# Optimization experiments

Measured on AMD Instinct MI355X. Metric: run time of the kernel, lower is better.

## Reference

```python
import jax, jax.numpy as jnp
import numpy as np

T = 32768       # sequence length (batch=1 in original forward)
DY = 63         # mark dim; input_size = DY + 1 = 64
D_IN = 64
H = 256         # hidden_size
OUT = 32        # out_size
NI = 1024       # number of inducing points


def _lstm_scan(x, w_ih, w_hh, b_ih, b_hh, reverse):
    """Single-direction LSTM over [T, D] input, batch=1. PyTorch gate order i,f,g,o."""
    xg = x @ w_ih.T + (b_ih + b_hh)  # [T, 4H], input projection precomputed

    def step(carry, xg_t):
        h, c = carry
        g = xg_t + h @ w_hh.T
        i, f, gg, o = jnp.split(g, 4)
        c = jax.nn.sigmoid(f) * c + jax.nn.sigmoid(i) * jnp.tanh(gg)
        h = jax.nn.sigmoid(o) * jnp.tanh(c)
        return (h, c), h

    init = (jnp.zeros((H,), x.dtype), jnp.zeros((H,), x.dtype))
    _, hs = jax.lax.scan(step, init, xg, reverse=reverse)
    return hs  # [T, H]


def _bilstm(x, layer_params):
    for (wf, uf, bif, bhf, wb, ub, bib, bhb) in layer_params:
        hf = _lstm_scan(x, wf, uf, bif, bhf, False)
        hb = _lstm_scan(x, wb, ub, bib, bhb, True)
        x = jnp.concatenate([hf, hb], axis=-1)  # [T, 2H]
    return x


def setup_inputs() -> dict:
    key = jax.random.key(0)
    ks = iter(jax.random.split(key, 24))
    s = 1.0 / np.sqrt(H)  # PyTorch LSTM uniform(-1/sqrt(H), 1/sqrt(H)) init
    def U(shape):
        return jax.random.uniform(next(ks), shape, jnp.float32, -s, s)
    inp = {
        "Y": jax.random.normal(next(ks), (T, DY), jnp.float32),
        "dT": jax.random.uniform(next(ks), (T,), jnp.float32),
        "induce_idx": jnp.sort(jax.random.randint(next(ks), (NI,), 0, T)),
        # layer 0: input D_IN; layer 1: input 2H (bidirectional)
        "w_ih_l0f": U((4 * H, D_IN)), "w_hh_l0f": U((4 * H, H)), "b_ih_l0f": U((4 * H,)), "b_hh_l0f": U((4 * H,)),
        "w_ih_l0b": U((4 * H, D_IN)), "w_hh_l0b": U((4 * H, H)), "b_ih_l0b": U((4 * H,)), "b_hh_l0b": U((4 * H,)),
        "w_ih_l1f": U((4 * H, 2 * H)), "w_hh_l1f": U((4 * H, H)), "b_ih_l1f": U((4 * H,)), "b_hh_l1f": U((4 * H,)),
        "w_ih_l1b": U((4 * H, 2 * H)), "w_hh_l1b": U((4 * H, H)), "b_ih_l1b": U((4 * H,)), "b_hh_l1b": U((4 * H,)),
        "fc_weight": jax.random.normal(next(ks), (2 * H, 2 * OUT), jnp.float32),
    }
    return inp


def reference(Y, dT, induce_idx,
              w_ih_l0f, w_hh_l0f, b_ih_l0f, b_hh_l0f,
              w_ih_l0b, w_hh_l0b, b_ih_l0b, b_hh_l0b,
              w_ih_l1f, w_hh_l1f, b_ih_l1f, b_hh_l1f,
              w_ih_l1b, w_hh_l1b, b_ih_l1b, b_hh_l1b,
              fc_weight):
    x = jnp.concatenate([Y, dT[:, None]], axis=1)  # [T, D_IN]
    layer_params = [
        (w_ih_l0f, w_hh_l0f, b_ih_l0f, b_hh_l0f, w_ih_l0b, w_hh_l0b, b_ih_l0b, b_hh_l0b),
        (w_ih_l1f, w_hh_l1f, b_ih_l1f, b_hh_l1f, w_ih_l1b, w_hh_l1b, b_ih_l1b, b_hh_l1b),
    ]
    h = _bilstm(x, layer_params)          # [T, 2H]
    out = h @ fc_weight                    # [T, 2*OUT]
    sel = out[induce_idx]                  # [NI, 2*OUT]
    return sel[:, :OUT], sel[:, OUT:]
```

## Files before the change

### kernel.cpp

```cpp
#include <hip/hip_runtime.h>

typedef unsigned int u32;
typedef unsigned short u16;
typedef _Float16 f16;
typedef _Float16 f16x2 __attribute__((ext_vector_type(2)));

#define T_SEQ 32768

static const size_t OFF_DT   = 0;
static const size_t OFF_FLG  = 1024;
static const size_t OFF_MAP  = 4096;
static const size_t OFF_H1G  = 135168;
static const size_t OFF_BIAS = 1183744;
static const size_t OFF_FCW  = 1200128;
static const size_t OFF_WQ8  = 1331200;
static const size_t OFF_WIH0 = 3428352;
static const size_t OFF_WIH1 = 3690496;
static const size_t OFF_XQ   = 5787648;
static const size_t OFF_H0   = 9981952;
static const size_t OFF_XG   = 43536384;
static const size_t XG_DIR   = (size_t)T_SEQ * 1024 * 2;
static const size_t NEED_PAR = OFF_XG + 2 * XG_DIR;

__device__ __forceinline__ float bf2f(u16 u) {
  union { u32 i; float f; } v; v.i = ((u32)u) << 16; return v.f;
}
__device__ __forceinline__ u16 f2bf(float f) {
  union { float f; u32 i; } v; v.f = f;
  u32 u = v.i;
  return (u16)((u + 0x7fffu + ((u >> 16) & 1u)) >> 16);
}
__device__ __forceinline__ u32 packf2(float a, float b) {
  f16x2 p; p.x = (f16)a; p.y = (f16)b;
  return __builtin_bit_cast(u32, p);
}
__device__ __forceinline__ u32 bf2f2(u32 v) {
  union { u32 i; float f; } lo, hi;
  lo.i = v << 16; hi.i = v & 0xffff0000u;
  return packf2(lo.f, hi.f);
}
__device__ __forceinline__ float ldf(const void* p, size_t i, u32 isf) {
  return isf ? ((const float*)p)[i] : bf2f(((const u16*)p)[i]);
}
__device__ __forceinline__ float fdot2f(f16x2 a, f16x2 b, float c) {
#if __has_builtin(__builtin_amdgcn_fdot2)
  return __builtin_amdgcn_fdot2(a, b, c, false);
#else
  return c + (float)a.x * (float)b.x + (float)a.y * (float)b.y;
#endif
}
__device__ __forceinline__ float fdotu(u32 a, u32 b, float c) {
  return fdot2f(__builtin_bit_cast(f16x2, a), __builtin_bit_cast(f16x2, b), c);
}
__device__ __forceinline__ int sdot4(u32 a, u32 b, int c) {
#if __has_builtin(__builtin_amdgcn_sdot4)
  return __builtin_amdgcn_sdot4((int)a, (int)b, c, false);
#else
  int r = c;
#pragma unroll
  for (int j = 0; j < 4; ++j)
    r += (int)(signed char)(a >> (8 * j)) * (int)(signed char)(b >> (8 * j));
  return r;
#endif
}
__device__ __forceinline__ int dpp_xor1(int x) {
#if __has_builtin(__builtin_amdgcn_update_dpp)
  return __builtin_amdgcn_update_dpp(0, x, 0xB1, 0xF, 0xF, true);
#else
  return __shfl_xor(x, 1);
#endif
}
__device__ __forceinline__ float sigf(float x) {
  return __builtin_amdgcn_rcpf(1.0f + __builtin_amdgcn_exp2f(-1.4426950408889634f * x));
}
__device__ __forceinline__ float tanhf_fast(float x) {
  return 1.0f - 2.0f * __builtin_amdgcn_rcpf(1.0f + __builtin_amdgcn_exp2f(2.8853900817779268f * x));
}

__global__ void k_detect(const u16* __restrict__ probe, u32* __restrict__ dt) {
  __shared__ int cnt;
  if (threadIdx.x == 0) cnt = 0;
  __syncthreads();
  int bad = 0;
  for (int i = threadIdx.x; i < 8192; i += 256) {
    float v = bf2f(probe[i]);
    if (!(v * v <= 16.0f)) bad++;
  }
  atomicAdd(&cnt, bad);
  __syncthreads();
  if (threadIdx.x == 0) *dt = (cnt > 64) ? 1u : 0u;
}

__global__ void k_conv_pairs(const void* __restrict__ src, u32* __restrict__ dst,
                             int np, const u32* __restrict__ dtp) {
  u32 isf = *dtp;
  int i = blockIdx.x * 256 + threadIdx.x;
  if (i >= np) return;
  if (isf) {
    const float* s = (const float*)src;
    dst[i] = packf2(s[2 * i], s[2 * i + 1]);
  } else {
    dst[i] = bf2f2(((const u32*)src)[i]);
  }
}

__global__ void k_quant(const void* __restrict__ src, u32* __restrict__ dst,
                        const u32* __restrict__ dtp) {
  u32 isf = *dtp;
  int i = blockIdx.x * 256 + threadIdx.x;
  int row = i >> 6, c = i & 63;
  u32 out = 0;
#pragma unroll
  for (int j = 0; j < 4; ++j) {
    float w = ldf(src, (size_t)row * 256 + 4 * c + j, isf);
    int q = (int)rintf(w * 2048.0f);
    q = q > 127 ? 127 : (q < -127 ? -127 : q);
    out |= ((u32)(q & 0xff)) << (8 * j);
  }
  dst[i] = out;
}

__global__ void k_conv_misc(const void* bi0f, const void* bh0f, const void* bi0b, const void* bh0b,
                            const void* bi1f, const void* bh1f, const void* bi1b, const void* bh1b,
                            const void* fcb, float* __restrict__ bias, float* __restrict__ fcw,
                            u32* __restrict__ flags, int* __restrict__ map,
                            const u32* __restrict__ dtp) {
  u32 isf = *dtp;
  int i = blockIdx.x * 256 + threadIdx.x;
  if (i < 4096) {
    int ld = i >> 10, r = i & 1023;
    const void* bi; const void* bh;
    if (ld == 0)      { bi = bi0f; bh = bh0f; }
    else if (ld == 1) { bi = bi0b; bh = bh0b; }
    else if (ld == 2) { bi = bi1f; bh = bh1f; }
    else              { bi = bi1b; bh = bh1b; }
    bias[i] = ldf(bi, r, isf) + ldf(bh, r, isf);
  } else if (i < 36864) {
    fcw[i - 4096] = ldf(fcb, i - 4096, isf);
  } else if (i < 36992) {
    flags[i - 36864] = 0;
  } else if (i < 69760) {
    map[i - 36992] = -1;
  }
}

__global__ void k_conv_x(const void* __restrict__ Y, const void* __restrict__ dT,
                         u32* __restrict__ xq, const u32* __restrict__ dtp) {
  u32 isf = *dtp;
  int i = blockIdx.x * 256 + threadIdx.x;
  if (i >= T_SEQ * 32) return;
  int t = i >> 5, m = i & 31, k2 = 2 * m;
  float a = ldf(Y, (size_t)t * 63 + k2, isf);
  float b = (k2 + 1 < 63) ? ldf(Y, (size_t)t * 63 + k2 + 1, isf) : ldf(dT, t, isf);
  xq[i] = packf2(a, b);
}

__global__ void k_map_set(const int* __restrict__ idx, int* __restrict__ map) {
  int i = blockIdx.x * 256 + threadIdx.x;
  if (i < 1024) map[idx[i]] = i;
}

__global__ __launch_bounds__(256) void k_gemm(
    const u32* __restrict__ Aq, const u32* __restrict__ Wc,
    const float* __restrict__ bias, f16* __restrict__ xg_slot, int Kp) {
  int t0 = blockIdx.x << 6, r0 = blockIdx.y << 6;
  int tid = threadIdx.x, tx = tid & 15, ty = tid >> 4;
  __shared__ u32 As[64][33];
  __shared__ u32 Bs[64][33];
  float acc[4][4] = {};
  for (int kp0 = 0; kp0 < Kp; kp0 += 32) {
#pragma unroll
    for (int i = 0; i < 8; ++i) {
      int idx = tid + (i << 8);
      int row = idx >> 5, kp = idx & 31, kpg = kp0 + kp;
      As[row][kp] = Aq[(size_t)(t0 + row) * Kp + kpg];
      Bs[row][kp] = Wc[(size_t)(r0 + row) * Kp + kpg];
    }
    __syncthreads();
#pragma unroll 4
    for (int kk = 0; kk < 32; ++kk) {
      u32 av[4], bv[4];
#pragma unroll
      for (int i = 0; i < 4; ++i) av[i] = As[ty * 4 + i][kk];
#pragma unroll
      for (int i = 0; i < 4; ++i) bv[i] = Bs[tx * 4 + i][kk];
#pragma unroll
      for (int i = 0; i < 4; ++i)
#pragma unroll
        for (int j = 0; j < 4; ++j)
          acc[i][j] = fdotu(av[i], bv[j], acc[i][j]);
    }
    __syncthreads();
  }
#pragma unroll
  for (int i = 0; i < 4; ++i) {
    int t = t0 + ty * 4 + i;
#pragma unroll
    for (int j = 0; j < 4; ++j) {
      int r = r0 + tx * 4 + j;
      xg_slot[(size_t)t * 1024 + r] = (f16)(acc[i][j] + bias[r]);
    }
  }
}

__global__ __launch_bounds__(512, 2) void k_recur2(
    const f16* __restrict__ xg, const u32* __restrict__ wq,
    f16* __restrict__ h_full, f16* __restrict__ h1g,
    const int* __restrict__ map, int dir0) {
  const int dir = dir0 + blockIdx.x;
  const int tid = threadIdx.x;
  const int u = tid >> 1;
  const int half = tid & 1;
  const u32* wqd = wq + ((size_t)dir << 16);

  __shared__ __align__(16) unsigned char hb8[2][256];

  u32 w0[32], w1[32], w2[32], w3[32];
  {
    const u32* p0 = wqd + ((size_t)(0 * 256 + u) << 6) + (half << 5);
    const u32* p1 = wqd + ((size_t)(1 * 256 + u) << 6) + (half << 5);
    const u32* p2 = wqd + ((size_t)(2 * 256 + u) << 6) + (half << 5);
    const u32* p3 = wqd + ((size_t)(3 * 256 + u) << 6) + (half << 5);
#pragma unroll
    for (int i = 0; i < 32; ++i) {
      w0[i] = p0[i]; w1[i] = p1[i]; w2[i] = p2[i]; w3[i] = p3[i];
    }
  }
#pragma unroll
  for (int i = 0; i < 32; ++i)
    asm volatile("" : "+v"(w0[i]), "+v"(w1[i]), "+v"(w2[i]), "+v"(w3[i]));

  if (tid < 128) ((u32*)hb8)[tid] = 0;

  float c_state = 0.f;
  const f16* xg_d = xg + ((size_t)blockIdx.x * T_SEQ * 1024);
  const float ksc = 1.0f / (2048.0f * 127.0f);

  int t = dir ? (T_SEQ - 1) : 0;
  float xa0 = (float)xg_d[(size_t)t * 1024 + u];
  float xa1 = (float)xg_d[(size_t)t * 1024 + 256 + u];
  float xa2 = (float)xg_d[(size_t)t * 1024 + 512 + u];
  float xa3 = (float)xg_d[(size_t)t * 1024 + 768 + u];
  int mp = map ? map[t] : -1;

  int p = 0;
  __syncthreads();

  for (int step = 0; step < T_SEQ; ++step) {
    float xb0 = xa0, xb1 = xa1, xb2 = xa2, xb3 = xa3;
    int ms = mp;
    const int tn = dir ? (T_SEQ - 2 - step) : (step + 1);
    if (step + 1 < T_SEQ) {
      xa0 = (float)xg_d[(size_t)tn * 1024 + u];
      xa1 = (float)xg_d[(size_t)tn * 1024 + 256 + u];
      xa2 = (float)xg_d[(size_t)tn * 1024 + 512 + u];
      xa3 = (float)xg_d[(size_t)tn * 1024 + 768 + u];
      if (map) mp = map[tn];
    }
    int acc0 = 0, acc1 = 0, acc2 = 0, acc3 = 0;
    const uint4* hp = (const uint4*)(&hb8[p][0]) + (half << 3);
#pragma unroll
    for (int c = 0; c < 8; ++c) {
      uint4 hv = hp[c];
      acc0 = sdot4(w0[4 * c + 0], hv.x, acc0);
      acc1 = sdot4(w1[4 * c + 0], hv.x, acc1);
      acc2 = sdot4(w2[4 * c + 0], hv.x, acc2);
      acc3 = sdot4(w3[4 * c + 0], hv.x, acc3);
      acc0 = sdot4(w0[4 * c + 1], hv.y, acc0);
      acc1 = sdot4(w1[4 * c + 1], hv.y, acc1);
      acc2 = sdot4(w2[4 * c + 1], hv.y, acc2);
      acc3 = sdot4(w3[4 * c + 1], hv.y, acc3);
      acc0 = sdot4(w0[4 * c + 2], hv.z, acc0);
      acc1 = sdot4(w1[4 * c + 2], hv.z, acc1);
      acc2 = sdot4(w2[4 * c + 2], hv.z, acc2);
      acc3 = sdot4(w3[4 * c + 2], hv.z, acc3);
      acc0 = sdot4(w0[4 * c + 3], hv.w, acc0);
      acc1 = sdot4(w1[4 * c + 3], hv.w, acc1);
      acc2 = sdot4(w2[4 * c + 3], hv.w, acc2);
      acc3 = sdot4(w3[4 * c + 3], hv.w, acc3);
    }
    acc0 += dpp_xor1(acc0);
    acc1 += dpp_xor1(acc1);
    acc2 += dpp_xor1(acc2);
    acc3 += dpp_xor1(acc3);
    float gi = sigf(xb0 + (float)acc0 * ksc);
    float gf = sigf(xb1 + (float)acc1 * ksc);
    float gg = tanhf_fast(xb2 + (float)acc2 * ksc);
    float go = sigf(xb3 + (float)acc3 * ksc);
    c_state = gf * c_state + gi * gg;
    float h = go * tanhf_fast(c_state);
    int q = (int)rintf(h * 127.0f);
    if (!half) {
      hb8[p ^ 1][u] = (unsigned char)(q & 0xff);
      if (h_full) h_full[(size_t)t * 512 + (dir << 8) + u] = (f16)h;
      if (h1g && ms >= 0) h1g[(size_t)ms * 512 + (dir << 8) + u] = (f16)h;
    }
    __syncthreads();
    p ^= 1;
    t = tn;
  }
}

__global__ void k_fc(const f16* __restrict__ h1g, const int* __restrict__ map,
                     const int* __restrict__ idx, const float* __restrict__ fcw,
                     void* __restrict__ out, const u32* __restrict__ dtp) {
  u32 isf = *dtp;
  int n = blockIdx.x;
  int cc = threadIdx.x;
  int slot = map[idx[n]];
  const f16* hp = h1g + (size_t)slot * 512;
  float acc = 0.f;
#pragma unroll 8
  for (int k = 0; k < 512; ++k) acc += (float)hp[k] * fcw[k * 64 + cc];
  int o = (cc < 32) ? (n * 32 + cc) : (32 * 1024 + n * 32 + (cc - 32));
  if (isf) ((float*)out)[o] = acc;
  else     ((u16*)out)[o]   = f2bf(acc);
}

extern "C" void kernel_launch(void* const* d_in, const int* in_sizes, int n_in,
                              void* d_out, int out_size, void* d_ws, size_t ws_size,
                              hipStream_t stream) {
  const void* Y        = d_in[0];
  const void* dT       = d_in[1];
  const int*  idx      = (const int*)d_in[2];
  const void* w_ih_l0f = d_in[3];
  const void* w_hh_l0f = d_in[4];
  const void* b_ih_l0f = d_in[5];
  const void* b_hh_l0f = d_in[6];
  const void* w_ih_l0b = d_in[7];
  const void* w_hh_l0b = d_in[8];
  const void* b_ih_l0b = d_in[9];
  const void* b_hh_l0b = d_in[10];
  const void* w_ih_l1f = d_in[11];
  const void* w_hh_l1f = d_in[12];
  const void* b_ih_l1f = d_in[13];
  const void* b_hh_l1f = d_in[14];
  const void* w_ih_l1b = d_in[15];
  const void* w_hh_l1b = d_in[16];
  const void* b_ih_l1b = d_in[17];
  const void* b_hh_l1b = d_in[18];
  const void* fcbf     = d_in[19];

  char* ws = (char*)d_ws;
  u32*  dt    = (u32*)(ws + OFF_DT);
  u32*  flags = (u32*)(ws + OFF_FLG);
  int*  map   = (int*)(ws + OFF_MAP);
  f16*  h1g   = (f16*)(ws + OFF_H1G);
  float* bias = (float*)(ws + OFF_BIAS);
  float* fcw  = (float*)(ws + OFF_FCW);
  u32*  wq8   = (u32*)(ws + OFF_WQ8);
  u32*  wih0  = (u32*)(ws + OFF_WIH0);
  u32*  wih1  = (u32*)(ws + OFF_WIH1);
  u32*  xq    = (u32*)(ws + OFF_XQ);
  f16*  h0    = (f16*)(ws + OFF_H0);
  f16*  xg    = (f16*)(ws + OFF_XG);
  f16*  xg1   = xg + XG_DIR / 2;

  const int par = (ws_size >= NEED_PAR) ? 1 : 0;

  k_detect<<<1, 256, 0, stream>>>((const u16*)w_hh_l0f, dt);
  k_quant<<<256, 256, 0, stream>>>(w_hh_l0f, wq8 + 0 * 65536, dt);
  k_quant<<<256, 256, 0, stream>>>(w_hh_l0b, wq8 + 1 * 65536, dt);
  k_quant<<<256, 256, 0, stream>>>(w_hh_l1f, wq8 + 2 * 65536, dt);
  k_quant<<<256, 256, 0, stream>>>(w_hh_l1b, wq8 + 3 * 65536, dt);
  k_conv_pairs<<<128, 256, 0, stream>>>(w_ih_l0f, wih0 + 0, 32768, dt);
  k_conv_pairs<<<128, 256, 0, stream>>>(w_ih_l0b, wih0 + 32768, 32768, dt);
  k_conv_pairs<<<1024, 256, 0, stream>>>(w_ih_l1f, wih1 + 0, 262144, dt);
  k_conv_pairs<<<1024, 256, 0, stream>>>(w_ih_l1b, wih1 + 262144, 262144, dt);
  k_conv_misc<<<273, 256, 0, stream>>>(b_ih_l0f, b_hh_l0f, b_ih_l0b, b_hh_l0b,
                                       b_ih_l1f, b_hh_l1f, b_ih_l1b, b_hh_l1b,
                                       fcbf, bias, fcw, flags, map, dt);
  k_conv_x<<<4096, 256, 0, stream>>>(Y, dT, xq, dt);
  k_map_set<<<4, 256, 0, stream>>>(idx, map);

  dim3 ggrid(T_SEQ / 64, 16);
  if (par) {
    k_gemm<<<ggrid, 256, 0, stream>>>(xq, wih0, bias, xg, 32);
    k_gemm<<<ggrid, 256, 0, stream>>>(xq, wih0 + 32768, bias + 1024, xg1, 32);
    k_recur2<<<2, 512, 0, stream>>>(xg, wq8, h0, nullptr, nullptr, 0);
    k_gemm<<<ggrid, 256, 0, stream>>>((const u32*)h0, wih1, bias + 2048, xg, 256);
    k_gemm<<<ggrid, 256, 0, stream>>>((const u32*)h0, wih1 + 262144, bias + 3072, xg1, 256);
    k_recur2<<<2, 512, 0, stream>>>(xg, wq8 + 2 * 65536, nullptr, h1g, map, 0);
  } else {
    k_gemm<<<ggrid, 256, 0, stream>>>(xq, wih0, bias, xg, 32);
    k_recur2<<<1, 512, 0, stream>>>(xg, wq8, h0, nullptr, nullptr, 0);
    k_gemm<<<ggrid, 256, 0, stream>>>(xq, wih0 + 32768, bias + 1024, xg, 32);
    k_recur2<<<1, 512, 0, stream>>>(xg, wq8, h0, nullptr, nullptr, 1);
    k_gemm<<<ggrid, 256, 0, stream>>>((const u32*)h0, wih1, bias + 2048, xg, 256);
    k_recur2<<<1, 512, 0, stream>>>(xg, wq8 + 2 * 65536, nullptr, h1g, map, 0);
    k_gemm<<<ggrid, 256, 0, stream>>>((const u32*)h0, wih1 + 262144, bias + 3072, xg, 256);
    k_recur2<<<1, 512, 0, stream>>>(xg, wq8 + 2 * 65536, nullptr, h1g, map, 1);
  }
  k_fc<<<1024, 64, 0, stream>>>(h1g, map, idx, fcw, d_out, dt);
}
```

Baseline: 62.21 ms.

## Split each LSTM hidden unit's recurrent dot product across four lanes

```diff
diff --git a/kernel.cpp b/kernel.cpp
--- a/kernel.cpp
+++ b/kernel.cpp
@@ -68,6 +68,13 @@
   return __builtin_amdgcn_update_dpp(0, x, 0xB1, 0xF, 0xF, true);
 #else
   return __shfl_xor(x, 1);
+#endif
+}
+__device__ __forceinline__ int dpp_xor2(int x) {
+#if __has_builtin(__builtin_amdgcn_update_dpp)
+  return __builtin_amdgcn_update_dpp(0, x, 0x4E, 0xF, 0xF, true);
+#else
+  return __shfl_xor(x, 2);
 #endif
 }
 __device__ __forceinline__ float sigf(float x) {
@@ -203,31 +210,37 @@
   }
 }
 
-__global__ __launch_bounds__(512, 2) void k_recur2(
+__global__ __launch_bounds__(1024, 4) void k_recur2(
     const f16* __restrict__ xg, const u32* __restrict__ wq,
     f16* __restrict__ h_full, f16* __restrict__ h1g,
     const int* __restrict__ map, int dir0) {
   const int dir = dir0 + blockIdx.x;
   const int tid = threadIdx.x;
-  const int u = tid >> 1;
-  const int half = tid & 1;
+  const int u = tid >> 2;
+  const int qq = tid & 3;
   const u32* wqd = wq + ((size_t)dir << 16);
 
   __shared__ __align__(16) unsigned char hb8[2][256];
 
-  u32 w0[32], w1[32], w2[32], w3[32];
+  u32 w0[16], w1[16], w2[16], w3[16];
   {
-    const u32* p0 = wqd + ((size_t)(0 * 256 + u) << 6) + (half << 5);
-    const u32* p1 = wqd + ((size_t)(1 * 256 + u) << 6) + (half << 5);
-    const u32* p2 = wqd + ((size_t)(2 * 256 + u) << 6) + (half << 5);
-    const u32* p3 = wqd + ((size_t)(3 * 256 + u) << 6) + (half << 5);
-#pragma unroll
-    for (int i = 0; i < 32; ++i) {
-      w0[i] = p0[i]; w1[i] = p1[i]; w2[i] = p2[i]; w3[i] = p3[i];
-    }
-  }
-#pragma unroll
-  for (int i = 0; i < 32; ++i)
+    const uint4* pw = (const uint4*)wqd;
+    const int b0 = ((0 << 8) | u) * 16 + (qq << 2);
+    const int b1 = ((1 << 8) | u) * 16 + (qq << 2);
+    const int b2 = ((2 << 8) | u) * 16 + (qq << 2);
+    const int b3 = ((3 << 8) | u) * 16 + (qq << 2);
+#pragma unroll
+    for (int i = 0; i < 4; ++i) {
+      uint4 v0 = pw[b0 + i]; uint4 v1 = pw[b1 + i];
+      uint4 v2 = pw[b2 + i]; uint4 v3 = pw[b3 + i];
+      w0[4 * i] = v0.x; w0[4 * i + 1] = v0.y; w0[4 * i + 2] = v0.z; w0[4 * i + 3] = v0.w;
+      w1[4 * i] = v1.x; w1[4 * i + 1] = v1.y; w1[4 * i + 2] = v1.z; w1[4 * i + 3] = v1.w;
+      w2[4 * i] = v2.x; w2[4 * i + 1] = v2.y; w2[4 * i + 2] = v2.z; w2[4 * i + 3] = v2.w;
+      w3[4 * i] = v3.x; w3[4 * i + 1] = v3.y; w3[4 * i + 2] = v3.z; w3[4 * i + 3] = v3.w;
+    }
+  }
+#pragma unroll
+  for (int i = 0; i < 16; ++i)
     asm volatile("" : "+v"(w0[i]), "+v"(w1[i]), "+v"(w2[i]), "+v"(w3[i]));
 
   if (tid < 128) ((u32*)hb8)[tid] = 0;
@@ -258,40 +271,43 @@
       if (map) mp = map[tn];
     }
     int acc0 = 0, acc1 = 0, acc2 = 0, acc3 = 0;
-    const uint4* hp = (const uint4*)(&hb8[p][0]) + (half << 3);
-#pragma unroll
-    for (int c = 0; c < 8; ++c) {
-      uint4 hv = hp[c];
-      acc0 = sdot4(w0[4 * c + 0], hv.x, acc0);
-      acc1 = sdot4(w1[4 * c + 0], hv.x, acc1);
-      acc2 = sdot4(w2[4 * c + 0], hv.x, acc2);
-      acc3 = sdot4(w3[4 * c + 0], hv.x, acc3);
-      acc0 = sdot4(w0[4 * c + 1], hv.y, acc0);
-      acc1 = sdot4(w1[4 * c + 1], hv.y, acc1);
-      acc2 = sdot4(w2[4 * c + 1], hv.y, acc2);
-      acc3 = sdot4(w3[4 * c + 1], hv.y, acc3);
-      acc0 = sdot4(w0[4 * c + 2], hv.z, acc0);
-      acc1 = sdot4(w1[4 * c + 2], hv.z, acc1);
-      acc2 = sdot4(w2[4 * c + 2], hv.z, acc2);
-      acc3 = sdot4(w3[4 * c + 2], hv.z, acc3);
-      acc0 = sdot4(w0[4 * c + 3], hv.w, acc0);
-      acc1 = sdot4(w1[4 * c + 3], hv.w, acc1);
-      acc2 = sdot4(w2[4 * c + 3], hv.w, acc2);
-      acc3 = sdot4(w3[4 * c + 3], hv.w, acc3);
-    }
-    acc0 += dpp_xor1(acc0);
-    acc1 += dpp_xor1(acc1);
-    acc2 += dpp_xor1(acc2);
-    acc3 += dpp_xor1(acc3);
+    const uint4* hp = (const uint4*)(&hb8[p][qq << 6]);
+    uint4 hv0 = hp[0], hv1 = hp[1], hv2 = hp[2], hv3 = hp[3];
+#define DOT16(HV, B)                                   \
+    acc0 = sdot4(w0[B],     HV.x, acc0);               \
+    acc1 = sdot4(w1[B],     HV.x, acc1);               \
+    acc2 = sdot4(w2[B],     HV.x, acc2);               \
+    acc3 = sdot4(w3[B],     HV.x, acc3);               \
+    acc0 = sdot4(w0[B + 1], HV.y, acc0);               \
+    acc1 = sdot4(w1[B + 1], HV.y, acc1);               \
+    acc2 = sdot4(w2[B + 1], HV.y, acc2);               \
+    acc3 = sdot4(w3[B + 1], HV.y, acc3);               \
+    acc0 = sdot4(w0[B + 2], HV.z, acc0);               \
+    acc1 = sdot4(w1[B + 2], HV.z, acc1);               \
+    acc2 = sdot4(w2[B + 2], HV.z, acc2);               \
+    acc3 = sdot4(w3[B + 2], HV.z, acc3);               \
+    acc0 = sdot4(w0[B + 3], HV.w, acc0);               \
+    acc1 = sdot4(w1[B + 3], HV.w, acc1);               \
+    acc2 = sdot4(w2[B + 3], HV.w, acc2);               \
+    acc3 = sdot4(w3[B + 3], HV.w, acc3);
+    DOT16(hv0, 0)
+    DOT16(hv1, 4)
+    DOT16(hv2, 8)
+    DOT16(hv3, 12)
+#undef DOT16
+    acc0 += dpp_xor1(acc0); acc0 += dpp_xor2(acc0);
+    acc1 += dpp_xor1(acc1); acc1 += dpp_xor2(acc1);
+    acc2 += dpp_xor1(acc2); acc2 += dpp_xor2(acc2);
+    acc3 += dpp_xor1(acc3); acc3 += dpp_xor2(acc3);
     float gi = sigf(xb0 + (float)acc0 * ksc);
     float gf = sigf(xb1 + (float)acc1 * ksc);
     float gg = tanhf_fast(xb2 + (float)acc2 * ksc);
     float go = sigf(xb3 + (float)acc3 * ksc);
     c_state = gf * c_state + gi * gg;
     float h = go * tanhf_fast(c_state);
-    int q = (int)rintf(h * 127.0f);
-    if (!half) {
-      hb8[p ^ 1][u] = (unsigned char)(q & 0xff);
+    int q8 = (int)rintf(h * 127.0f);
+    if (qq == 0) {
+      hb8[p ^ 1][u] = (unsigned char)(q8 & 0xff);
       if (h_full) h_full[(size_t)t * 512 + (dir << 8) + u] = (f16)h;
       if (h1g && ms >= 0) h1g[(size_t)ms * 512 + (dir << 8) + u] = (f16)h;
     }
@@ -377,19 +393,19 @@
   if (par) {
     k_gemm<<<ggrid, 256, 0, stream>>>(xq, wih0, bias, xg, 32);
     k_gemm<<<ggrid, 256, 0, stream>>>(xq, wih0 + 32768, bias + 1024, xg1, 32);
-    k_recur2<<<2, 512, 0, stream>>>(xg, wq8, h0, nullptr, nullptr, 0);
+    k_recur2<<<2, 1024, 0, stream>>>(xg, wq8, h0, nullptr, nullptr, 0);
     k_gemm<<<ggrid, 256, 0, stream>>>((const u32*)h0, wih1, bias + 2048, xg, 256);
     k_gemm<<<ggrid, 256, 0, stream>>>((const u32*)h0, wih1 + 262144, bias + 3072, xg1, 256);
-    k_recur2<<<2, 512, 0, stream>>>(xg, wq8 + 2 * 65536, nullptr, h1g, map, 0);
+    k_recur2<<<2, 1024, 0, stream>>>(xg, wq8 + 2 * 65536, nullptr, h1g, map, 0);
   } else {
     k_gemm<<<ggrid, 256, 0, stream>>>(xq, wih0, bias, xg, 32);
-    k_recur2<<<1, 512, 0, stream>>>(xg, wq8, h0, nullptr, nullptr, 0);
+    k_recur2<<<1, 1024, 0, stream>>>(xg, wq8, h0, nullptr, nullptr, 0);
     k_gemm<<<ggrid, 256, 0, stream>>>(xq, wih0 + 32768, bias + 1024, xg, 32);
-    k_recur2<<<1, 512, 0, stream>>>(xg, wq8, h0, nullptr, nullptr, 1);
+    k_recur2<<<1, 1024, 0, stream>>>(xg, wq8, h0, nullptr, nullptr, 1);
     k_gemm<<<ggrid, 256, 0, stream>>>((const u32*)h0, wih1, bias + 2048, xg, 256);
-    k_recur2<<<1, 512, 0, stream>>>(xg, wq8 + 2 * 65536, nullptr, h1g, map, 0);
+    k_recur2<<<1, 1024, 0, stream>>>(xg, wq8 + 2 * 65536, nullptr, h1g, map, 0);
     k_gemm<<<ggrid, 256, 0, stream>>>((const u32*)h0, wih1 + 262144, bias + 3072, xg, 256);
-    k_recur2<<<1, 512, 0, stream>>>(xg, wq8 + 2 * 65536, nullptr, h1g, map, 1);
+    k_recur2<<<1, 1024, 0, stream>>>(xg, wq8 + 2 * 65536, nullptr, h1g, map, 1);
   }
   k_fc<<<1024, 64, 0, stream>>>(h1g, map, idx, fcw, d_out, dt);
 }
```

Measured after the change: 76.75 ms. +23.4%, slower.
